# Optimization experiments

Hardware: AMD Instinct MI355X
Metric: run time of the kernel (lower is better)

The kernel has to match this reference:

```python
import jax, jax.numpy as jnp
import numpy as np

B, S, C, H = 2, 2048, 2048, 16
Dh = C // H
ROPE_THETA = 10000.0


def _rope(t):
    # t: [B, S, H, Dh]; rotate-half RoPE over head_dim
    half = Dh // 2
    inv_freq = 1.0 / (ROPE_THETA ** (jnp.arange(0, half, dtype=jnp.float32) / half))
    ang = jnp.arange(S, dtype=jnp.float32)[:, None] * inv_freq[None, :]  # [S, half]
    cos = jnp.cos(ang)[None, :, None, :]  # [1,S,1,half]
    sin = jnp.sin(ang)[None, :, None, :]
    t1, t2 = t[..., :half], t[..., half:]
    return jnp.concatenate([t1 * cos - t2 * sin, t2 * cos + t1 * sin], axis=-1)


def setup_inputs() -> dict:
    key = jax.random.key(0)
    k1, k2, k3 = jax.random.split(key, 3)
    x = jax.random.normal(k1, (B, S, C), dtype=jnp.float32)
    Wqkv = jax.random.normal(k2, (C, 3 * C), dtype=jnp.float32) * (C ** -0.5)
    Wproj = jax.random.normal(k3, (C, C), dtype=jnp.float32) * (C ** -0.5)
    return {"x": x, "Wqkv": Wqkv, "Wproj": Wproj}


def reference(x, Wqkv, Wproj):
    batch, seq, hidden = x.shape
    qkv = x @ Wqkv  # [B,S,3C]
    # NOTE: torch code chunks as k, q, v (k first)
    k, q, v = jnp.split(qkv, 3, axis=-1)
    k = k.reshape(batch, seq, H, Dh)
    q = q.reshape(batch, seq, H, Dh)
    v = v.reshape(batch, seq, H, Dh)
    k = _rope(k)
    q = _rope(q)
    scale = Dh ** -0.5
    scores = jnp.einsum('bqhd,bkhd->bhqk', q, k) * scale  # [B,H,S,S]
    causal = jnp.tril(jnp.ones((seq, seq), dtype=bool))
    scores = jnp.where(causal[None, None], scores, jnp.finfo(scores.dtype).min)
    attn = jax.nn.softmax(scores, axis=-1)
    out = jnp.einsum('bhqk,bkhd->bqhd', attn, v).reshape(batch, seq, hidden)
    return out @ Wproj
```

## Files before the change

### kernel.cpp

```cpp
#include <hip/hip_runtime.h>
#include <hip/hip_bf16.h>

#define B_   2
#define S_   2048
#define C_   2048
#define H_   16
#define DH   128
#define C3   (3 * C_)

typedef __attribute__((ext_vector_type(8))) short short8;
typedef __attribute__((ext_vector_type(4))) float floatx4;

__device__ __forceinline__ void gload16(const void* g, void* l) {
  __builtin_amdgcn_global_load_lds(
      (const __attribute__((address_space(1))) unsigned int*)g,
      (__attribute__((address_space(3))) unsigned int*)l, 16, 0, 0);
}

__device__ __forceinline__ unsigned pk_bf16(float a, float b) {
  union { __hip_bfloat16 h; unsigned short u; } ua, ub;
  ua.h = __float2bfloat16(a); ub.h = __float2bfloat16(b);
  return (unsigned)ua.u | ((unsigned)ub.u << 16);
}

__device__ __forceinline__ float bf2f(short u) {
  union { unsigned u; float f; } t;
  t.u = ((unsigned)(unsigned short)u) << 16;
  return t.f;
}
__device__ __forceinline__ short f2bf(float f) {
  union { __hip_bfloat16 h; short s; } t;
  t.h = __float2bfloat16(f);
  return t.s;
}

__device__ __forceinline__ void transpose_cast_dev(
    const float* __restrict__ in, __hip_bfloat16* __restrict__ out,
    int R, int Cc, int c0, int r0, int tid, float (*tile)[33]) {
  int tx = tid & 31, ty = tid >> 5;
#pragma unroll
  for (int k = 0; k < 4; ++k)
    tile[ty + 8 * k][tx] = in[(size_t)(r0 + ty + 8 * k) * Cc + c0 + tx];
  __syncthreads();
#pragma unroll
  for (int k = 0; k < 4; ++k)
    out[(size_t)(c0 + ty + 8 * k) * R + r0 + tx] = __float2bfloat16(tile[tx][ty + 8 * k]);
}

__global__ __launch_bounds__(256) void pre_kernel(
    const float* __restrict__ x, __hip_bfloat16* __restrict__ xb,
    const float* __restrict__ Wqkv, __hip_bfloat16* __restrict__ WqkvT) {
  __shared__ float tile[32][33];
  const int bid = blockIdx.x, tid = threadIdx.x;
  if (bid < 8192) {
    int i = bid * 256 + tid;
    float4 v = ((const float4*)x)[i];
    union { __hip_bfloat16 b[4]; uint2 u; } t;
    t.b[0] = __float2bfloat16(v.x);
    t.b[1] = __float2bfloat16(v.y);
    t.b[2] = __float2bfloat16(v.z);
    t.b[3] = __float2bfloat16(v.w);
    ((uint2*)xb)[i] = t.u;
  } else {
    int tb = bid - 8192;
    int bx = tb % 192, by = tb / 192;
    transpose_cast_dev(Wqkv, WqkvT, 2048, 6144, bx * 32, by * 32, tid, tile);
  }
}

#define S_VMCNT2 do { asm volatile("s_waitcnt vmcnt(2)" ::: "memory"); \
                      __builtin_amdgcn_sched_barrier(0); } while (0)
#define S_LGKM0  do { asm volatile("s_waitcnt lgkmcnt(0)" ::: "memory"); \
                      __builtin_amdgcn_sched_barrier(0); } while (0)
#define S_BAR    do { __builtin_amdgcn_s_barrier(); \
                      __builtin_amdgcn_sched_barrier(0); } while (0)

#define RD_A4(dst, buf, mh, sl)                                                          \
  do {                                                                                   \
    const __hip_bfloat16* base_ =                                                        \
        lds + (buf) * 28672 + (wm * 128 + (mh) * 64 + lr) * 64 + ((sl) ? sw1 : sw0);     \
    _Pragma("unroll") for (int i_ = 0; i_ < 4; ++i_)                                     \
        dst[i_] = *(const short8*)(base_ + i_ * 1024);                                   \
  } while (0)

#define RD_B3(dst, buf, sl)                                                              \
  do {                                                                                   \
    const __hip_bfloat16* base_ =                                                        \
        lds + (buf) * 28672 + 16384 + (wn * 48 + lr) * 64 + ((sl) ? sw1 : sw0);          \
    _Pragma("unroll") for (int j_ = 0; j_ < 3; ++j_)                                     \
        dst[j_] = *(const short8*)(base_ + j_ * 1024);                                   \
  } while (0)

#define MFG(afp, bfp, mh)                                                                \
  do {                                                                                   \
    __builtin_amdgcn_s_setprio(1);                                                       \
    _Pragma("unroll") for (int i_ = 0; i_ < 4; ++i_)                                     \
    _Pragma("unroll") for (int j_ = 0; j_ < 3; ++j_)                                     \
        acc[(mh) * 4 + i_][j_] = __builtin_amdgcn_mfma_f32_16x16x32_bf16(                \
            afp[i_], bfp[j_], acc[(mh) * 4 + i_][j_], 0, 0, 0);                          \
    __builtin_amdgcn_s_setprio(0);                                                       \
  } while (0)

__global__ __launch_bounds__(512, 2) void gemm1_kernel(
    const __hip_bfloat16* __restrict__ A, const __hip_bfloat16* __restrict__ Bt,
    __hip_bfloat16* __restrict__ Cp) {
  const int K = 2048;
  __shared__ __hip_bfloat16 lds[2 * 28672];
  const int tid = threadIdx.x;
  const int lane = tid & 63, wv = tid >> 6;
  const int wm = wv >> 2, wn = wv & 3;
  const int lr = lane & 15, lq = lane >> 4;
  const int m0 = blockIdx.y * 256, n0 = blockIdx.x * 192;
  const int sw0 = (lq ^ (lr & 7)) << 3;
  const int sw1 = sw0 ^ 32;

  const __hip_bfloat16* Abase = A + (size_t)m0 * K;
  const __hip_bfloat16* Bbase = Bt + (size_t)n0 * K;

  auto stA = [&](int buf, int half, int kk) {
#pragma unroll
    for (int pp = 0; pp < 2; ++pp) {
      int p = half * 2 + pp;
      int idx = p * 512 + tid;
      int row = idx >> 3;
      int lc = (idx & 7) ^ (row & 7);
      gload16(Abase + (size_t)row * K + kk + lc * 8,
              (char*)lds + buf * 57344 + p * 8192 + wv * 1024);
    }
  };
  auto stB2 = [&](int buf, int kk) {
#pragma unroll
    for (int p = 0; p < 2; ++p) {
      int idx = p * 512 + tid;
      int row = idx >> 3;
      int lc = (idx & 7) ^ (row & 7);
      gload16(Bbase + (size_t)row * K + kk + lc * 8,
              (char*)lds + buf * 57344 + 32768 + p * 8192 + wv * 1024);
    }
  };
  auto stB1 = [&](int buf, int kk) {
    int idx = 2 * 512 + tid;
    int row = idx >> 3;
    int lc = (idx & 7) ^ (row & 7);
    gload16(Bbase + (size_t)row * K + kk + lc * 8,
            (char*)lds + buf * 57344 + 49152 + wv * 1024);
  };

  floatx4 acc[8][3] = {};
  short8 afA[4], afB[4], afC[4], afD[4], bfA[3], bfB[3];

  stA(0, 0, 0); stA(0, 1, 0); stB2(0, 0); stB1(0, 0);
  stA(1, 0, 64);

#pragma unroll 1
  for (int it = 0; it < 16; ++it) {
    const int t = 2 * it;
    const int kk1 = (t + 1) * 64;
    const int kk2 = (t + 2 < 32) ? (t + 2) * 64 : 0;
    const int kk3 = (t + 3 < 32) ? (t + 3) * 64 : 0;

    S_VMCNT2; S_BAR;
    RD_A4(afA, 0, 0, 0); RD_B3(bfA, 0, 0);
    stA(1, 1, kk1);
    S_LGKM0;
    MFG(afA, bfA, 0);
    S_BAR;
    RD_A4(afB, 0, 1, 0); RD_A4(afC, 0, 0, 1);
    stB2(1, kk1);
    S_LGKM0;
    MFG(afB, bfA, 1);
    S_BAR;
    RD_B3(bfB, 0, 1); RD_A4(afD, 0, 1, 1);
    stB1(1, kk1);
    S_LGKM0;
    MFG(afC, bfB, 0);
    S_BAR;
    stA(0, 0, kk2);
    MFG(afD, bfB, 1);
    S_BAR;

    S_VMCNT2; S_BAR;
    RD_A4(afA, 1, 0, 0); RD_B3(bfA, 1, 0);
    stA(0, 1, kk2);
    S_LGKM0;
    MFG(afA, bfA, 0);
    S_BAR;
    RD_A4(afB, 1, 1, 0); RD_A4(afC, 1, 0, 1);
    stB2(0, kk2);
    S_LGKM0;
    MFG(afB, bfA, 1);
    S_BAR;
    RD_B3(bfB, 1, 1); RD_A4(afD, 1, 1, 1);
    stB1(0, kk2);
    S_LGKM0;
    MFG(afC, bfB, 0);
    S_BAR;
    stA(1, 0, kk3);
    MFG(afD, bfB, 1);
    S_BAR;
  }

  asm volatile("s_waitcnt vmcnt(0)" ::: "memory");
  __builtin_amdgcn_sched_barrier(0);

#pragma unroll
  for (int i = 0; i < 8; ++i)
#pragma unroll
    for (int j = 0; j < 3; ++j)
#pragma unroll
      for (int r = 0; r < 4; ++r) {
        int row = m0 + wm * 128 + i * 16 + lq * 4 + r;
        int col = n0 + wn * 48 + j * 16 + lr;
        Cp[(size_t)row * 6144 + col] = __float2bfloat16(acc[i][j][r]);
      }
}

#define S_VMCNT6 do { asm volatile("s_waitcnt vmcnt(6)" ::: "memory"); \
                      __builtin_amdgcn_sched_barrier(0); } while (0)

template <int NCOLS, bool OUT_F32>
__global__ __launch_bounds__(512, 2) void gemm_dp_kernel(
    const __hip_bfloat16* __restrict__ A, const __hip_bfloat16* __restrict__ Bt,
    void* __restrict__ Cp) {
  const int K = 2048, NT = 32;
  __shared__ __hip_bfloat16 lds[3 * 24576];
  const int tid = threadIdx.x;
  const int lane = tid & 63, wv = tid >> 6;
  const int wm = wv >> 1, wn = wv & 1;
  const int lr = lane & 15, lq = lane >> 4;
  const int m0 = blockIdx.y * 256, n0 = blockIdx.x * 128;
  const int sw0 = (lq ^ (lr & 7)) << 3;
  const int sw1 = sw0 ^ 32;

  auto stageA = [&](int bw, int p, int kk) {
    int idx = p * 512 + tid;
    int row = idx >> 3;
    int lc = (idx & 7) ^ (row & 7);
    gload16(A + (size_t)(m0 + row) * K + kk + lc * 8,
            (char*)lds + (size_t)bw * 49152 + (size_t)(p * 512 + wv * 64) * 16);
  };
  auto stageB = [&](int bw, int p, int kk) {
    int idx = p * 512 + tid;
    int row = idx >> 3;
    int lc = (idx & 7) ^ (row & 7);
    gload16(Bt + (size_t)(n0 + row) * K + kk + lc * 8,
            (char*)lds + (size_t)bw * 49152 + 32768 + (size_t)(p * 512 + wv * 64) * 16);
  };

#pragma unroll
  for (int p = 0; p < 4; ++p) stageA(0, p, 0);
#pragma unroll
  for (int p = 0; p < 2; ++p) stageB(0, p, 0);
#pragma unroll
  for (int p = 0; p < 4; ++p) stageA(1, p, 64);
#pragma unroll
  for (int p = 0; p < 2; ++p) stageB(1, p, 64);

  floatx4 acc[4][4] = {};
  int br = 0, bw = 2;

#pragma unroll 1
  for (int t = 0; t < NT; ++t) {
    const int kk2 = (t + 2 < NT) ? (t + 2) * 64 : 0;

    S_VMCNT6;
    S_BAR;

    const __hip_bfloat16* Ab = lds + br * 24576 + (wm * 64 + lr) * 64;
    const __hip_bfloat16* Bb = lds + br * 24576 + 16384 + (wn * 64 + lr) * 64;

    short8 af0[4], bf0[4];
#pragma unroll
    for (int i = 0; i < 4; ++i) af0[i] = *(const short8*)(Ab + i * 1024 + sw0);
#pragma unroll
    for (int j = 0; j < 4; ++j) bf0[j] = *(const short8*)(Bb + j * 1024 + sw0);
    stageA(bw, 0, kk2); stageA(bw, 1, kk2); stageB(bw, 0, kk2);
    S_LGKM0;
    __builtin_amdgcn_s_setprio(1);
#pragma unroll
    for (int i = 0; i < 4; ++i)
#pragma unroll
      for (int j = 0; j < 4; ++j)
        acc[i][j] = __builtin_amdgcn_mfma_f32_16x16x32_bf16(af0[i], bf0[j], acc[i][j], 0, 0, 0);
    __builtin_amdgcn_s_setprio(0);

    short8 af1[4], bf1[4];
#pragma unroll
    for (int i = 0; i < 4; ++i) af1[i] = *(const short8*)(Ab + i * 1024 + sw1);
#pragma unroll
    for (int j = 0; j < 4; ++j) bf1[j] = *(const short8*)(Bb + j * 1024 + sw1);
    stageA(bw, 2, kk2); stageA(bw, 3, kk2); stageB(bw, 1, kk2);
    S_LGKM0;
    __builtin_amdgcn_s_setprio(1);
#pragma unroll
    for (int i = 0; i < 4; ++i)
#pragma unroll
      for (int j = 0; j < 4; ++j)
        acc[i][j] = __builtin_amdgcn_mfma_f32_16x16x32_bf16(af1[i], bf1[j], acc[i][j], 0, 0, 0);
    __builtin_amdgcn_s_setprio(0);

    br = (br == 2) ? 0 : br + 1;
    bw = (bw == 2) ? 0 : bw + 1;
  }

  asm volatile("s_waitcnt vmcnt(0)" ::: "memory");
  __builtin_amdgcn_sched_barrier(0);

#pragma unroll
  for (int i = 0; i < 4; ++i)
#pragma unroll
    for (int j = 0; j < 4; ++j)
#pragma unroll
      for (int r = 0; r < 4; ++r) {
        int row = m0 + wm * 64 + i * 16 + lq * 4 + r;
        int col = n0 + wn * 64 + j * 16 + lr;
        if (OUT_F32)
          ((float*)Cp)[(size_t)row * NCOLS + col] = acc[i][j][r];
        else
          ((__hip_bfloat16*)Cp)[(size_t)row * NCOLS + col] = __float2bfloat16(acc[i][j][r]);
      }
}

__global__ __launch_bounds__(256) void mid_kernel(
    __hip_bfloat16* __restrict__ qkv, __hip_bfloat16* __restrict__ vt,
    const float* __restrict__ Wproj, __hip_bfloat16* __restrict__ WprojT) {
  __shared__ char smem[18432];
  const int bid = blockIdx.x, tid = threadIdx.x;

  if (bid < 2048) {
    int i = bid * 256 + tid;
    int d8 = (i & 7) << 3;
    int h = (i >> 3) & 15;
    int row = i >> 7;
    int s = row & (S_ - 1);
    size_t base = (size_t)row * C3 + h * DH + d8;
    short8 k1 = *(const short8*)(qkv + base);
    short8 k2 = *(const short8*)(qkv + base + 64);
    short8 q1 = *(const short8*)(qkv + base + C_);
    short8 q2 = *(const short8*)(qkv + base + C_ + 64);
    short8 ko1, ko2, qo1, qo2;
    const float scale = 0.08838834764831845f * 1.4426950408889634f;
#pragma unroll
    for (int j = 0; j < 8; ++j) {
      float invf = exp2f((float)(d8 + j) * (-13.287712379549449f / 64.0f));
      float ang = (float)s * invf;
      float sn, c;
      __sincosf(ang, &sn, &c);
      float a = bf2f(k1[j]), b = bf2f(k2[j]);
      ko1[j] = f2bf(a * c - b * sn);
      ko2[j] = f2bf(b * c + a * sn);
      a = bf2f(q1[j]); b = bf2f(q2[j]);
      qo1[j] = f2bf((a * c - b * sn) * scale);
      qo2[j] = f2bf((b * c + a * sn) * scale);
    }
    *(short8*)(qkv + base) = ko1;
    *(short8*)(qkv + base + 64) = ko2;
    *(short8*)(qkv + base + C_) = qo1;
    *(short8*)(qkv + base + C_ + 64) = qo2;
  } else if (bid < 3072) {
    short* T = (short*)smem;
    const int t = (bid - 2048) & 31, bh = (bid - 2048) >> 5;
    const int b = bh >> 4, h = bh & 15;
    const size_t brow = (size_t)b * S_;
#pragma unroll
    for (int p = 0; p < 4; ++p) {
      int idx = p * 256 + tid;
      int row = idx >> 4, c8 = idx & 15;
      *(short8*)(T + row * 144 + c8 * 8) =
          *(const short8*)(qkv + (brow + t * 64 + row) * C3 + 2 * C_ + h * DH + c8 * 8);
    }
    __syncthreads();
#pragma unroll
    for (int p = 0; p < 4; ++p) {
      int L = p * 256 + tid;
      int d = L & 127, cs = L >> 7;
      short8 v;
#pragma unroll
      for (int j = 0; j < 8; ++j) v[j] = T[(cs * 8 + j) * 144 + d];
      *(short8*)(vt + ((size_t)bh * 32 + t) * 8192 + (size_t)L * 8) = v;
    }
  } else {
    int tb = bid - 3072;
    int bx = tb & 63, by = tb >> 6;
    transpose_cast_dev(Wproj, WprojT, 2048, 2048, bx * 32, by * 32, tid,
                       (float(*)[33])smem);
  }
}

__global__ __launch_bounds__(256, 2) void attn_kernel(
    const __hip_bfloat16* __restrict__ qkv,
    const __hip_bfloat16* __restrict__ vt_tiles,
    __hip_bfloat16* __restrict__ outp) {
  __shared__ __hip_bfloat16 Ks[64 * 128];
  __shared__ __hip_bfloat16 Vt[64 * 128];
  __shared__ __hip_bfloat16 Ps[4 * 32 * 72];

  const int tid = threadIdx.x, lane = tid & 63, wv = tid >> 6;
  const int lr = lane & 15, lq = lane >> 4;
  const int n = blockIdx.y * 16 + blockIdx.x;
  const int half = n >> 8, rr = n & 255;
  const int bh = rr >> 3, p = rr & 7;
  const int qt = half ? p : 15 - p;
  const int b = bh >> 4, h = bh & 15;
  const int q0 = qt * 128;
  const int q0w = q0 + wv * 32;
  const size_t brow = (size_t)b * S_;

  short8 qf[2][4];
#pragma unroll
  for (int rt = 0; rt < 2; ++rt)
#pragma unroll
    for (int ks = 0; ks < 4; ++ks)
      qf[rt][ks] = *(const short8*)(qkv + (brow + q0w + rt * 16 + lr) * C3 + C_ + h * DH + ks * 32 + lq * 8);

  floatx4 of[2][8] = {};
  float l_run[2] = {0.0f, 0.0f};

  const int wrow_last = q0w + 31;
  const int nkt = 2 * qt + 2;
  for (int kt = 0; kt < nkt; ++kt) {
    const int kb = kt * 64;
#pragma unroll
    for (int pp = 0; pp < 4; ++pp) {
      int L = pp * 256 + wv * 64 + lane;
      int srow = L >> 4;
      int ck = (L & 15) ^ (srow & 15);
      gload16(qkv + (brow + kb + srow) * C3 + h * DH + ck * 8,
              (char*)Ks + (size_t)(pp * 256 + wv * 64) * 16);
      gload16(vt_tiles + ((size_t)bh * 32 + kt) * 8192 + (size_t)L * 8,
              (char*)Vt + (size_t)(pp * 256 + wv * 64) * 16);
    }
    __syncthreads();

    if (kb <= wrow_last) {
      floatx4 st[2][4] = {};
#pragma unroll
      for (int ks = 0; ks < 4; ++ks) {
        short8 kfr[4];
#pragma unroll
        for (int t4 = 0; t4 < 4; ++t4)
          kfr[t4] = *(const short8*)(Ks + ((t4 * 16 + lr) * 16 + ((ks * 4 + lq) ^ lr)) * 8);
#pragma unroll
        for (int rt = 0; rt < 2; ++rt)
#pragma unroll
          for (int t4 = 0; t4 < 4; ++t4)
            st[rt][t4] = __builtin_amdgcn_mfma_f32_16x16x32_bf16(kfr[t4], qf[rt][ks], st[rt][t4], 0, 0, 0);
      }

      if (kb + 63 > q0w) {
#pragma unroll
        for (int rt = 0; rt < 2; ++rt)
#pragma unroll
          for (int t4 = 0; t4 < 4; ++t4)
#pragma unroll
            for (int r = 0; r < 4; ++r) {
              int s = kb + t4 * 16 + lq * 4 + r;
              if (s > q0w + rt * 16 + lr) st[rt][t4][r] = -1e30f;
            }
      }

#pragma unroll
      for (int rt = 0; rt < 2; ++rt) {
        float rs = 0.0f;
#pragma unroll
        for (int t4 = 0; t4 < 4; ++t4)
#pragma unroll
          for (int r = 0; r < 4; ++r) {
            float pv = exp2f(st[rt][t4][r]);
            st[rt][t4][r] = pv;
            rs += pv;
          }
        rs += __shfl_xor(rs, 16);
        rs += __shfl_xor(rs, 32);
        l_run[rt] += rs;
      }

#pragma unroll
      for (int rt = 0; rt < 2; ++rt)
#pragma unroll
        for (int t4 = 0; t4 < 4; ++t4) {
          unsigned* pdst = (unsigned*)(Ps + (wv * 32 + rt * 16 + lr) * 72 + t4 * 16 + lq * 4);
          pdst[0] = pk_bf16(st[rt][t4][0], st[rt][t4][1]);
          pdst[1] = pk_bf16(st[rt][t4][2], st[rt][t4][3]);
        }

#pragma unroll
      for (int ks = 0; ks < 2; ++ks) {
        short8 pa[2];
#pragma unroll
        for (int rt = 0; rt < 2; ++rt)
          pa[rt] = *(const short8*)(Ps + (wv * 32 + rt * 16 + lr) * 72 + ks * 32 + lq * 8);
#pragma unroll
        for (int dt = 0; dt < 8; ++dt) {
          short8 vb = *(const short8*)(Vt + ((ks * 4 + lq) * 128 + dt * 16 + lr) * 8);
#pragma unroll
          for (int rt = 0; rt < 2; ++rt)
            of[rt][dt] = __builtin_amdgcn_mfma_f32_16x16x32_bf16(pa[rt], vb, of[rt][dt], 0, 0, 0);
        }
      }
    }
    __syncthreads();
  }

#pragma unroll
  for (int rt = 0; rt < 2; ++rt) {
    float linv = 1.0f / l_run[rt];
    floatx4 lv;
#pragma unroll
    for (int r = 0; r < 4; ++r) lv[r] = __shfl(linv, lq * 4 + r);
#pragma unroll
    for (int dt = 0; dt < 8; ++dt)
#pragma unroll
      for (int r = 0; r < 4; ++r)
        outp[(brow + q0w + rt * 16 + lq * 4 + r) * C_ + h * DH + dt * 16 + lr] =
            __float2bfloat16(of[rt][dt][r] * lv[r]);
  }
}

extern "C" void kernel_launch(void* const* d_in, const int* in_sizes, int n_in,
                              void* d_out, int out_size, void* d_ws, size_t ws_size,
                              hipStream_t stream) {
  const float* x = (const float*)d_in[0];
  const float* Wqkv = (const float*)d_in[1];
  const float* Wproj = (const float*)d_in[2];

  __hip_bfloat16* xb = (__hip_bfloat16*)d_ws;
  __hip_bfloat16* WqkvT = xb + (size_t)4096 * 2048;
  __hip_bfloat16* qkvb = WqkvT + (size_t)6144 * 2048;
  __hip_bfloat16* WprojT = WqkvT;
  __hip_bfloat16* vt_tiles = WqkvT + (size_t)2048 * 2048;
  __hip_bfloat16* attnb = xb;

  pre_kernel<<<8192 + 12288, 256, 0, stream>>>(x, xb, Wqkv, WqkvT);

  gemm1_kernel<<<dim3(6144 / 192, 4096 / 256), 512, 0, stream>>>(xb, WqkvT, qkvb);

  mid_kernel<<<2048 + 1024 + 4096, 256, 0, stream>>>(qkvb, vt_tiles, Wproj, WprojT);

  attn_kernel<<<dim3(16, 32), 256, 0, stream>>>(qkvb, vt_tiles, attnb);

  gemm_dp_kernel<2048, true><<<dim3(2048 / 128, 4096 / 256), 512, 0, stream>>>(
      attnb, WprojT, (float*)d_out);
}
```

Measured before the change: 347.0 us.

## Enlarge QKV GEMM tile to 512x192 with a triple-buffered A ring

Reworks the QKV projection GEMM so each 512-thread block computes a 512x192 output tile, with 8 waves arranged 4x2 and each wave owning a 128x96 subtile. A is streamed in 32-wide K slices through a three-stage LDS ring, and B is double buffered in 64-wide K slices. The goal is better reuse of operands per LDS read and fewer global loads per FLOP. The cost is a larger accumulator array (48 floatx4 per wave), which raises register pressure and could lower occupancy. The grid also shrinks to 256 blocks, which may underfill the 256 CUs given 2 blocks/CU bounds.

```diff
diff --git a/kernel.cpp b/kernel.cpp
--- a/kernel.cpp
+++ b/kernel.cpp
@@ -68,136 +68,104 @@
   }
 }
 
-#define S_VMCNT2 do { asm volatile("s_waitcnt vmcnt(2)" ::: "memory"); \
-                      __builtin_amdgcn_sched_barrier(0); } while (0)
 #define S_LGKM0  do { asm volatile("s_waitcnt lgkmcnt(0)" ::: "memory"); \
                       __builtin_amdgcn_sched_barrier(0); } while (0)
 #define S_BAR    do { __builtin_amdgcn_s_barrier(); \
                       __builtin_amdgcn_sched_barrier(0); } while (0)
-
-#define RD_A4(dst, buf, mh, sl)                                                          \
-  do {                                                                                   \
-    const __hip_bfloat16* base_ =                                                        \
-        lds + (buf) * 28672 + (wm * 128 + (mh) * 64 + lr) * 64 + ((sl) ? sw1 : sw0);     \
-    _Pragma("unroll") for (int i_ = 0; i_ < 4; ++i_)                                     \
-        dst[i_] = *(const short8*)(base_ + i_ * 1024);                                   \
-  } while (0)
-
-#define RD_B3(dst, buf, sl)                                                              \
-  do {                                                                                   \
-    const __hip_bfloat16* base_ =                                                        \
-        lds + (buf) * 28672 + 16384 + (wn * 48 + lr) * 64 + ((sl) ? sw1 : sw0);          \
-    _Pragma("unroll") for (int j_ = 0; j_ < 3; ++j_)                                     \
-        dst[j_] = *(const short8*)(base_ + j_ * 1024);                                   \
-  } while (0)
-
-#define MFG(afp, bfp, mh)                                                                \
+#define S_VMC(n) do { asm volatile("s_waitcnt vmcnt(" #n ")" ::: "memory"); \
+                      __builtin_amdgcn_sched_barrier(0); } while (0)
+
+
+#define MFMA24(ih)                                                                       \
   do {                                                                                   \
     __builtin_amdgcn_s_setprio(1);                                                       \
     _Pragma("unroll") for (int i_ = 0; i_ < 4; ++i_)                                     \
-    _Pragma("unroll") for (int j_ = 0; j_ < 3; ++j_)                                     \
-        acc[(mh) * 4 + i_][j_] = __builtin_amdgcn_mfma_f32_16x16x32_bf16(                \
-            afp[i_], bfp[j_], acc[(mh) * 4 + i_][j_], 0, 0, 0);                          \
+    _Pragma("unroll") for (int j_ = 0; j_ < 6; ++j_)                                     \
+        acc[(ih) * 4 + i_][j_] = __builtin_amdgcn_mfma_f32_16x16x32_bf16(                \
+            af[i_], bf[j_], acc[(ih) * 4 + i_][j_], 0, 0, 0);                            \
     __builtin_amdgcn_s_setprio(0);                                                       \
+  } while (0)
+
+#define G1_TILE(VMC_N, UPAR, KKA, KKB, DO_B)                                             \
+  do {                                                                                   \
+    S_VMC(VMC_N);                                                                        \
+    S_BAR;                                                                               \
+    const __hip_bfloat16* Ab = lds + rd * 16384 + aoff;                                  \
+    const __hip_bfloat16* Bb = lds + 49152 + (UPAR) * 12288 + boff +                     \
+                               ((((t_ & 1) * 4 + lq) ^ (lr & 7)) << 3);                  \
+    short8 af[4], bf[6];                                                                 \
+    _Pragma("unroll") for (int i_ = 0; i_ < 4; ++i_)                                     \
+        af[i_] = *(const short8*)(Ab + i_ * 512);                                        \
+    _Pragma("unroll") for (int j_ = 0; j_ < 6; ++j_)                                     \
+        bf[j_] = *(const short8*)(Bb + j_ * 1024);                                       \
+    stA(st, (KKA));                                                                      \
+    if (DO_B) stB(!(UPAR), (KKB));                                                       \
+    S_LGKM0;                                                                             \
+    MFMA24(0);                                                                           \
+    _Pragma("unroll") for (int i_ = 0; i_ < 4; ++i_)                                     \
+        af[i_] = *(const short8*)(Ab + 2048 + i_ * 512);                                 \
+    S_LGKM0;                                                                             \
+    MFMA24(1);                                                                           \
+    rd = (rd == 2) ? 0 : rd + 1;                                                         \
+    st = (st == 2) ? 0 : st + 1;                                                         \
   } while (0)
 
 __global__ __launch_bounds__(512, 2) void gemm1_kernel(
     const __hip_bfloat16* __restrict__ A, const __hip_bfloat16* __restrict__ Bt,
     __hip_bfloat16* __restrict__ Cp) {
   const int K = 2048;
-  __shared__ __hip_bfloat16 lds[2 * 28672];
+  __shared__ __hip_bfloat16 lds[73728];
   const int tid = threadIdx.x;
   const int lane = tid & 63, wv = tid >> 6;
-  const int wm = wv >> 2, wn = wv & 3;
+  const int wm = wv >> 1, wn = wv & 1;
   const int lr = lane & 15, lq = lane >> 4;
-  const int m0 = blockIdx.y * 256, n0 = blockIdx.x * 192;
-  const int sw0 = (lq ^ (lr & 7)) << 3;
-  const int sw1 = sw0 ^ 32;
+  const int m0 = blockIdx.y * 512, n0 = blockIdx.x * 192;
+  const int aoff = (wm * 128 + lr) * 32 + ((lq ^ ((lr >> 1) & 3)) << 3);
+  const int boff = (wn * 96 + lr) * 64;
 
   const __hip_bfloat16* Abase = A + (size_t)m0 * K;
   const __hip_bfloat16* Bbase = Bt + (size_t)n0 * K;
 
-  auto stA = [&](int buf, int half, int kk) {
-#pragma unroll
-    for (int pp = 0; pp < 2; ++pp) {
-      int p = half * 2 + pp;
+  auto stA = [&](int ring, int kk) {
+#pragma unroll
+    for (int p = 0; p < 4; ++p) {
       int idx = p * 512 + tid;
-      int row = idx >> 3;
-      int lc = (idx & 7) ^ (row & 7);
+      int row = idx >> 2;
+      int lc = (idx & 3) ^ ((row >> 1) & 3);
       gload16(Abase + (size_t)row * K + kk + lc * 8,
-              (char*)lds + buf * 57344 + p * 8192 + wv * 1024);
+              (char*)lds + ring * 32768 + p * 8192 + wv * 1024);
     }
   };
-  auto stB2 = [&](int buf, int kk) {
-#pragma unroll
-    for (int p = 0; p < 2; ++p) {
+  auto stB = [&](int buf, int kk) {
+#pragma unroll
+    for (int p = 0; p < 3; ++p) {
       int idx = p * 512 + tid;
       int row = idx >> 3;
       int lc = (idx & 7) ^ (row & 7);
       gload16(Bbase + (size_t)row * K + kk + lc * 8,
-              (char*)lds + buf * 57344 + 32768 + p * 8192 + wv * 1024);
+              (char*)lds + 98304 + buf * 24576 + p * 8192 + wv * 1024);
     }
   };
-  auto stB1 = [&](int buf, int kk) {
-    int idx = 2 * 512 + tid;
-    int row = idx >> 3;
-    int lc = (idx & 7) ^ (row & 7);
-    gload16(Bbase + (size_t)row * K + kk + lc * 8,
-            (char*)lds + buf * 57344 + 49152 + wv * 1024);
-  };
-
-  floatx4 acc[8][3] = {};
-  short8 afA[4], afB[4], afC[4], afD[4], bfA[3], bfB[3];
-
-  stA(0, 0, 0); stA(0, 1, 0); stB2(0, 0); stB1(0, 0);
-  stA(1, 0, 64);
-
+
+  floatx4 acc[8][6] = {};
+
+  stA(0, 0); stB(0, 0); stA(1, 32);
+
+  int rd = 0, st = 2;
 #pragma unroll 1
-  for (int it = 0; it < 16; ++it) {
-    const int t = 2 * it;
-    const int kk1 = (t + 1) * 64;
-    const int kk2 = (t + 2 < 32) ? (t + 2) * 64 : 0;
-    const int kk3 = (t + 3 < 32) ? (t + 3) * 64 : 0;
-
-    S_VMCNT2; S_BAR;
-    RD_A4(afA, 0, 0, 0); RD_B3(bfA, 0, 0);
-    stA(1, 1, kk1);
-    S_LGKM0;
-    MFG(afA, bfA, 0);
-    S_BAR;
-    RD_A4(afB, 0, 1, 0); RD_A4(afC, 0, 0, 1);
-    stB2(1, kk1);
-    S_LGKM0;
-    MFG(afB, bfA, 1);
-    S_BAR;
-    RD_B3(bfB, 0, 1); RD_A4(afD, 0, 1, 1);
-    stB1(1, kk1);
-    S_LGKM0;
-    MFG(afC, bfB, 0);
-    S_BAR;
-    stA(0, 0, kk2);
-    MFG(afD, bfB, 1);
-    S_BAR;
-
-    S_VMCNT2; S_BAR;
-    RD_A4(afA, 1, 0, 0); RD_B3(bfA, 1, 0);
-    stA(0, 1, kk2);
-    S_LGKM0;
-    MFG(afA, bfA, 0);
-    S_BAR;
-    RD_A4(afB, 1, 1, 0); RD_A4(afC, 1, 0, 1);
-    stB2(0, kk2);
-    S_LGKM0;
-    MFG(afB, bfA, 1);
-    S_BAR;
-    RD_B3(bfB, 1, 1); RD_A4(afD, 1, 1, 1);
-    stB1(0, kk2);
-    S_LGKM0;
-    MFG(afC, bfB, 0);
-    S_BAR;
-    stA(1, 0, kk3);
-    MFG(afD, bfB, 1);
-    S_BAR;
+  for (int u = 0; u < 32; ++u) {
+    const int t0 = 2 * u;
+    const int kkA2 = (t0 + 2 < 64) ? (t0 + 2) * 32 : 0;
+    const int kkA3 = (t0 + 3 < 64) ? (t0 + 3) * 32 : 0;
+    const int kkB  = (u + 1 < 32) ? (u + 1) * 64 : 0;
+    {
+      const int t_ = t0;
+      G1_TILE(4, (u & 1), kkA2, kkB, 1);
+    }
+    {
+      const int t_ = t0 + 1;
+      G1_TILE(7, (u & 1), kkA3, 0, 0);
+    }
   }
 
   asm volatile("s_waitcnt vmcnt(0)" ::: "memory");
@@ -206,11 +174,11 @@
 #pragma unroll
   for (int i = 0; i < 8; ++i)
 #pragma unroll
-    for (int j = 0; j < 3; ++j)
+    for (int j = 0; j < 6; ++j)
 #pragma unroll
       for (int r = 0; r < 4; ++r) {
         int row = m0 + wm * 128 + i * 16 + lq * 4 + r;
-        int col = n0 + wn * 48 + j * 16 + lr;
+        int col = n0 + wn * 96 + j * 16 + lr;
         Cp[(size_t)row * 6144 + col] = __float2bfloat16(acc[i][j][r]);
       }
 }
@@ -533,7 +501,7 @@
 
   pre_kernel<<<8192 + 12288, 256, 0, stream>>>(x, xb, Wqkv, WqkvT);
 
-  gemm1_kernel<<<dim3(6144 / 192, 4096 / 256), 512, 0, stream>>>(xb, WqkvT, qkvb);
+  gemm1_kernel<<<dim3(32, 8), 512, 0, stream>>>(xb, WqkvT, qkvb);
 
   mid_kernel<<<2048 + 1024 + 4096, 256, 0, stream>>>(qkvb, vt_tiles, Wproj, WprojT);
 
```

After: 357.7 us. 3.1% more time.
